# Kernel optimization log

Hardware: AMD Instinct MI355X
Metric: run time of the kernel (lower is better)

## Reference

```python
import jax, jax.numpy as jnp
import numpy as np

N_STEPS = 20      # max(n_steps_al, n_steps_kc)
ALPHA   = 0.9     # membrane decay exp(-dt/tau_m)
V_TH    = 1.0     # spiking threshold
G_SOMA  = 0.3     # dendrite->axon coupling conductance (2-compartment KC)
APL_GAIN = 1.0    # graded APL gain
I_SCALE = 0.5     # graded ORN drive scale
BETA    = 10.0    # surrogate-gradient sharpness ('soft' sigmoid)

@jax.custom_vjp
def spike(x):
    return (x > 0).astype(x.dtype)

def _spike_fwd(x):
    return spike(x), x

def _spike_bwd(x, g):
    s = jax.nn.sigmoid(BETA * x)
    return (g * BETA * s * (1.0 - s),)

spike.defvjp(_spike_fwd, _spike_bwd)


def _sparse_w(key, shape, density):
    k1, k2 = jax.random.split(key)
    mask = jax.random.bernoulli(k1, density, shape)
    w = jax.random.uniform(k2, shape)
    return (mask * w).astype(jnp.float32)


def setup_inputs() -> dict:
    key = jax.random.key(0)
    ks = jax.random.split(key, 10)
    batch, n_or, n_orn, n_ln, n_pn, n_kc, n_odors = 4096, 21, 42, 56, 42, 2000, 34
    or_input = jax.random.uniform(ks[0], (batch, n_or), dtype=jnp.float32)
    or_gains = jnp.ones((n_or,), jnp.float32)
    # fixed OR->ORN mapping: OR i drives left (2i) and right (2i+1) ORNs
    m = np.zeros((n_or, n_orn), np.float32)
    for i in range(n_or):
        m[i, 2 * i] = 1.0
        m[i, 2 * i + 1] = 1.0
    mapping = jnp.asarray(m)
    orn_to_pn = _sparse_w(ks[1], (n_orn, n_pn), 0.3)
    orn_to_ln = _sparse_w(ks[2], (n_orn, n_ln), 0.3)
    ln_to_pn = _sparse_w(ks[3], (n_ln, n_pn), 0.3)
    pn_to_kc = _sparse_w(ks[4], (n_pn, n_kc), 0.15)  # ~6 PN claws per KC
    kc_to_apl = jax.random.uniform(ks[5], (n_kc, 1), dtype=jnp.float32) * 0.01
    apl_to_kc = jax.random.uniform(ks[6], (1, n_kc), dtype=jnp.float32)
    dec_w = jax.random.normal(ks[7], (n_kc, n_odors), dtype=jnp.float32) * 0.02
    dec_b = jnp.zeros((n_odors,), jnp.float32)
    return {"or_input": or_input, "or_gains": or_gains, "mapping": mapping,
            "orn_to_pn": orn_to_pn, "orn_to_ln": orn_to_ln, "ln_to_pn": ln_to_pn,
            "pn_to_kc": pn_to_kc, "kc_to_apl": kc_to_apl, "apl_to_kc": apl_to_kc,
            "dec_w": dec_w, "dec_b": dec_b}


def reference(or_input, or_gains, mapping, orn_to_pn, orn_to_ln, ln_to_pn,
              pn_to_kc, kc_to_apl, apl_to_kc, dec_w, dec_b):
    B = or_input.shape[0]
    n_orn, n_pn = orn_to_pn.shape
    n_ln = orn_to_ln.shape[1]
    n_kc = pn_to_kc.shape[1]
    # OR transduction: graded, learnable per-OR gain
    orn_drive = (or_input * jax.nn.softplus(or_gains)) @ mapping  # [B, n_orn]

    z = lambda n: jnp.zeros((B, n), or_input.dtype)
    carry0 = (z(n_orn), z(n_ln), z(n_pn), z(n_kc), z(n_kc), z(1), z(n_kc))

    def step(carry, _):
        v_orn, v_ln, v_pn, v_d, v_a, apl, kc_cnt = carry
        # ORN LIF driven by graded OR current
        v_orn = ALPHA * v_orn + I_SCALE * orn_drive
        s_orn = spike(v_orn - V_TH)
        v_orn = v_orn * (1.0 - s_orn)
        # LN LIF (lateral inhibition interneurons)
        v_ln = ALPHA * v_ln + s_orn @ orn_to_ln
        s_ln = spike(v_ln - V_TH)
        v_ln = v_ln * (1.0 - s_ln)
        # PN LIF: ORN excitation, LN inhibition
        v_pn = ALPHA * v_pn + s_orn @ orn_to_pn - s_ln @ ln_to_pn
        s_pn = spike(v_pn - V_TH)
        v_pn = v_pn * (1.0 - s_pn)
        # KC 2-compartment: dendrite gets PN input and APL inhibition
        v_d = ALPHA * v_d + s_pn @ pn_to_kc - apl @ apl_to_kc
        v_a = ALPHA * v_a + G_SOMA * (v_d - v_a)
        s_kc = spike(v_a - V_TH)
        v_a = v_a * (1.0 - s_kc)
        # APL: graded (non-spiking) global inhibition from KC spikes
        apl = APL_GAIN * jax.nn.relu(s_kc @ kc_to_apl)
        return (v_orn, v_ln, v_pn, v_d, v_a, apl, kc_cnt + s_kc), None

    carry, _ = jax.lax.scan(step, carry0, None, length=N_STEPS)
    kc_count = carry[-1]
    kc_rates = kc_count / N_STEPS
    logits = kc_rates @ dec_w + dec_b  # [B, n_odors]
    return logits
```

## Files before the change

### kernel.cpp

```cpp
#include <hip/hip_runtime.h>

#define NSTEPS 20
#define ALPHA  0.9f
#define VTH    1.0f
#define GSOMA  0.3f
#define ISCALE 0.5f

#define NOR  21
#define NORN 42
#define NLN  56
#define NPN  42
#define NKC  2000
#define NOD  34

#define TPB  256
#define KPER 8

__global__ __launch_bounds__(TPB)
void phase1_sparse(const float* __restrict__ or_input,
                   const float* __restrict__ or_gains,
                   const float* __restrict__ mapping,
                   const float* __restrict__ orn_to_ln,
                   const float* __restrict__ orn_to_pn,
                   const float* __restrict__ ln_to_pn,
                   unsigned long long* __restrict__ gPN,
                   int batch)
{
    __shared__ float sOl[NORN * NLN];
    __shared__ float sOp[NORN * NPN];
    __shared__ float sLp[NLN * NPN];

    const int tid = threadIdx.x;
    for (int i = tid; i < NORN * NLN; i += TPB) sOl[i] = orn_to_ln[i];
    for (int i = tid; i < NORN * NPN; i += TPB) sOp[i] = orn_to_pn[i];
    for (int i = tid; i < NLN * NPN;  i += TPB) sLp[i] = ln_to_pn[i];
    __syncthreads();

    const int lane = tid & 63;
    const int wid  = tid >> 6;
    const int row  = blockIdx.x * 4 + wid;
    if (row >= batch) return;

    float spg = 0.f;
    if (lane < NOR) spg = log1pf(expf(or_gains[lane]));

    float drive = 0.f;
    {
        const float* x = or_input + (long)row * NOR;
        const int jo = lane < NORN ? lane : 0;
#pragma unroll
        for (int i = 0; i < NOR; ++i) {
            float g = __shfl(spg, i);
            drive += x[i] * g * mapping[i * NORN + jo];
        }
        drive *= ISCALE;
    }

    const int jl = lane < NLN ? lane : 0;
    const int jp = lane < NPN ? lane : 0;

    float v_orn = 0.f, v_ln = 0.f, v_pn = 0.f;
    unsigned long long* outm = gPN + (long)row * NSTEPS;

    for (int t = 0; t < NSTEPS; ++t) {
        bool so = false;
        if (lane < NORN) {
            v_orn = ALPHA * v_orn + drive;
            so = (v_orn - VTH) > 0.f;
            if (so) v_orn = 0.f;
        }
        unsigned long long mO = __ballot(so);

        float aln = 0.f, apn = 0.f;
        {
            unsigned long long m = mO;
            while (m) {
                const int p = __builtin_ctzll(m);
                m &= m - 1;
                aln += sOl[p * NLN + jl];
                apn += sOp[p * NPN + jp];
            }
        }

        bool sl = false;
        if (lane < NLN) {
            v_ln = ALPHA * v_ln + aln;
            sl = (v_ln - VTH) > 0.f;
            if (sl) v_ln = 0.f;
        }
        unsigned long long mL = __ballot(sl);

        float h = 0.f;
        {
            unsigned long long m = mL;
            while (m) {
                const int l = __builtin_ctzll(m);
                m &= m - 1;
                h += sLp[l * NPN + jp];
            }
        }

        bool sp = false;
        if (lane < NPN) {
            v_pn = ALPHA * v_pn + apn - h;
            sp = (v_pn - VTH) > 0.f;
            if (sp) v_pn = 0.f;
        }
        const unsigned long long mP = __ballot(sp);
        if (lane == 0) outm[t] = mP;
    }
}

__global__ __launch_bounds__(TPB)
void phase2_kernel(const unsigned long long* __restrict__ g_masks,
                   const float* __restrict__ pn_to_kc,
                   const float* __restrict__ kc_to_apl,
                   const float* __restrict__ apl_to_kc,
                   const float* __restrict__ dec_w,
                   const float* __restrict__ dec_b,
                   float* __restrict__ out)
{
    __shared__ float sRed[2][4];
    __shared__ float sRed2[4 * NOD];

    const int tid  = threadIdx.x;
    const int lane = tid & 63;
    const int wid  = tid >> 6;
    const int b    = blockIdx.x;

    const int  kbase = tid * KPER;
    const bool act   = (kbase < NKC);
    float vd[KPER], va[KPER], cnt[KPER], wa2k[KPER], wk2a[KPER];
#pragma unroll
    for (int j = 0; j < KPER; ++j) { vd[j] = 0.f; va[j] = 0.f; cnt[j] = 0.f; }
    {
        const float4* a4 = (const float4*)(apl_to_kc + (act ? kbase : 0));
        const float4* k4 = (const float4*)(kc_to_apl + (act ? kbase : 0));
        float4 a0 = a4[0], a1 = a4[1], k0 = k4[0], k1 = k4[1];
        const float g = act ? 1.f : 0.f;
        wa2k[0] = g * a0.x; wa2k[1] = g * a0.y; wa2k[2] = g * a0.z; wa2k[3] = g * a0.w;
        wa2k[4] = g * a1.x; wa2k[5] = g * a1.y; wa2k[6] = g * a1.z; wa2k[7] = g * a1.w;
        wk2a[0] = g * k0.x; wk2a[1] = g * k0.y; wk2a[2] = g * k0.z; wk2a[3] = g * k0.w;
        wk2a[4] = g * k1.x; wk2a[5] = g * k1.y; wk2a[6] = g * k1.z; wk2a[7] = g * k1.w;
    }
    if (tid < 8) sRed[tid >> 2][tid & 3] = 0.f;
    __syncthreads();

    const unsigned long long* gm = g_masks + (long)b * NSTEPS;

    for (int t = 0; t < NSTEPS; ++t) {
        const float* rp = sRed[(t + 1) & 1];
        const float apl = fmaxf(rp[0] + rp[1] + rp[2] + rp[3], 0.f);

#pragma unroll
        for (int j = 0; j < KPER; ++j) vd[j] = ALPHA * vd[j] - apl * wa2k[j];

        unsigned long long m = gm[t];
        while (m) {
            const int p0 = __builtin_ctzll(m); m &= m - 1;
            int p1 = p0; float f1 = 0.f;
            if (m) { p1 = __builtin_ctzll(m); m &= m - 1; f1 = 1.f; }
            if (act) {
                const float4* w0 = (const float4*)(pn_to_kc + (long)p0 * NKC + kbase);
                const float4* w1 = (const float4*)(pn_to_kc + (long)p1 * NKC + kbase);
                float4 a0 = w0[0], a1 = w0[1];
                float4 b0 = w1[0], b1 = w1[1];
                vd[0] += a0.x; vd[1] += a0.y; vd[2] += a0.z; vd[3] += a0.w;
                vd[4] += a1.x; vd[5] += a1.y; vd[6] += a1.z; vd[7] += a1.w;
                vd[0] += f1 * b0.x; vd[1] += f1 * b0.y; vd[2] += f1 * b0.z; vd[3] += f1 * b0.w;
                vd[4] += f1 * b1.x; vd[5] += f1 * b1.y; vd[6] += f1 * b1.z; vd[7] += f1 * b1.w;
            }
        }

        float aplp = 0.f;
#pragma unroll
        for (int j = 0; j < KPER; ++j) {
            va[j] = ALPHA * va[j] + GSOMA * (vd[j] - va[j]);
            float s = (va[j] - VTH) > 0.f ? 1.f : 0.f;
            va[j] *= (1.f - s);
            cnt[j] += s;
            aplp += s * wk2a[j];
        }
        for (int off = 32; off > 0; off >>= 1) aplp += __shfl_xor(aplp, off, 64);
        if (lane == 0) sRed[t & 1][wid] = aplp;
        __syncthreads();
    }

    float acc[NOD];
#pragma unroll
    for (int o = 0; o < NOD; ++o) acc[o] = 0.f;
    if (act) {
#pragma unroll
        for (int j = 0; j < KPER; ++j) {
            float r = cnt[j] / 20.0f;
            if (r != 0.f) {
                const float* wr = dec_w + (long)(kbase + j) * NOD;
#pragma unroll
                for (int o = 0; o < NOD; ++o) acc[o] += r * wr[o];
            }
        }
    }
#pragma unroll
    for (int o = 0; o < NOD; ++o) {
        float v = acc[o];
        for (int off = 32; off > 0; off >>= 1) v += __shfl_xor(v, off, 64);
        if (lane == 0) sRed2[wid * NOD + o] = v;
    }
    __syncthreads();
    if (tid < NOD) {
        float v = sRed2[tid] + sRed2[NOD + tid] + sRed2[2 * NOD + tid] +
                  sRed2[3 * NOD + tid] + dec_b[tid];
        out[(long)b * NOD + tid] = v;
    }
}

__global__ __launch_bounds__(TPB)
void snn_fused(const float* __restrict__ or_input, const float* __restrict__ or_gains,
               const float* __restrict__ mapping, const float* __restrict__ orn_to_pn,
               const float* __restrict__ orn_to_ln, const float* __restrict__ ln_to_pn,
               const float* __restrict__ pn_to_kc, const float* __restrict__ kc_to_apl,
               const float* __restrict__ apl_to_kc, const float* __restrict__ dec_w,
               const float* __restrict__ dec_b, float* __restrict__ out)
{
    __shared__ float sW_ol[NORN * NLN];
    __shared__ float sW_op[NORN * NPN];
    __shared__ float sW_lp[NLN * NPN];
    __shared__ float sDrive[NORN];
    __shared__ float sSpg[NOR];
    __shared__ float sOrn[NORN];
    __shared__ float sLn[NLN];
    __shared__ float sApl;
    __shared__ float sRed[4];
    __shared__ float sRed2[4 * NOD];
    __shared__ unsigned long long sMask;

    const int tid = threadIdx.x;
    const int b   = blockIdx.x;

    for (int i = tid; i < NORN * NLN; i += TPB) sW_ol[i] = orn_to_ln[i];
    for (int i = tid; i < NORN * NPN; i += TPB) sW_op[i] = orn_to_pn[i];
    for (int i = tid; i < NLN * NPN;  i += TPB) sW_lp[i] = ln_to_pn[i];
    if (tid < NOR) sSpg[tid] = log1pf(expf(or_gains[tid]));
    if (tid == 0)  sApl = 0.f;
    __syncthreads();

    if (tid < NORN) {
        const float* x = or_input + (long)b * NOR;
        float d = 0.f;
        for (int i = 0; i < NOR; ++i) d += x[i] * sSpg[i] * mapping[i * NORN + tid];
        sDrive[tid] = d * ISCALE;
    }

    const int  kbase = tid * KPER;
    const bool act   = (kbase < NKC);
    float vd[KPER], va[KPER], cnt[KPER], wa2k[KPER], wk2a[KPER];
#pragma unroll
    for (int j = 0; j < KPER; ++j) {
        vd[j] = 0.f; va[j] = 0.f; cnt[j] = 0.f;
        wa2k[j] = act ? apl_to_kc[kbase + j] : 0.f;
        wk2a[j] = act ? kc_to_apl[kbase + j] : 0.f;
    }
    float v_orn = 0.f, v_ln = 0.f, v_pn = 0.f, v_pn_exc = 0.f;
    __syncthreads();

    for (int t = 0; t < NSTEPS; ++t) {
        if (tid < NORN) {
            v_orn = ALPHA * v_orn + sDrive[tid];
            float s = (v_orn - VTH) > 0.f ? 1.f : 0.f;
            v_orn *= (1.f - s);
            sOrn[tid] = s;
        }
        __syncthreads();
        if (tid < NLN) {
            float a = 0.f;
            for (int o = 0; o < NORN; ++o) a += sOrn[o] * sW_ol[o * NLN + tid];
            v_ln = ALPHA * v_ln + a;
            float s = (v_ln - VTH) > 0.f ? 1.f : 0.f;
            v_ln *= (1.f - s);
            sLn[tid] = s;
        } else if (tid >= 64 && tid < 64 + NPN) {
            const int j = tid - 64;
            float a = 0.f;
            for (int o = 0; o < NORN; ++o) a += sOrn[o] * sW_op[o * NPN + j];
            v_pn_exc = a;
        }
        __syncthreads();
        if (tid >= 64 && tid < 64 + NPN) {
            const int j = tid - 64;
            float inh = 0.f;
            for (int l = 0; l < NLN; ++l) inh += sLn[l] * sW_lp[l * NPN + j];
            v_pn = ALPHA * v_pn + v_pn_exc - inh;
            bool s = (v_pn - VTH) > 0.f;
            if (s) v_pn = 0.f;
            unsigned long long bal = __ballot(s);
            if (tid == 64) sMask = bal;
        }
        __syncthreads();
        {
            const float apl = sApl;
#pragma unroll
            for (int j = 0; j < KPER; ++j) vd[j] = ALPHA * vd[j] - apl * wa2k[j];
            unsigned long long m = sMask;
            while (m) {
                const int p = __builtin_ctzll(m);
                m &= m - 1;
                if (act) {
                    const float4* w = (const float4*)(pn_to_kc + (long)p * NKC + kbase);
                    float4 w0 = w[0], w1 = w[1];
                    vd[0] += w0.x; vd[1] += w0.y; vd[2] += w0.z; vd[3] += w0.w;
                    vd[4] += w1.x; vd[5] += w1.y; vd[6] += w1.z; vd[7] += w1.w;
                }
            }
            float aplp = 0.f;
#pragma unroll
            for (int j = 0; j < KPER; ++j) {
                va[j] = ALPHA * va[j] + GSOMA * (vd[j] - va[j]);
                float s = (va[j] - VTH) > 0.f ? 1.f : 0.f;
                va[j] *= (1.f - s);
                cnt[j] += s;
                aplp += s * wk2a[j];
            }
            for (int off = 32; off > 0; off >>= 1) aplp += __shfl_xor(aplp, off, 64);
            if ((tid & 63) == 0) sRed[tid >> 6] = aplp;
        }
        __syncthreads();
        if (tid == 0) {
            float a = sRed[0] + sRed[1] + sRed[2] + sRed[3];
            sApl = fmaxf(a, 0.f);
        }
    }

    float acc[NOD];
#pragma unroll
    for (int o = 0; o < NOD; ++o) acc[o] = 0.f;
    if (act) {
#pragma unroll
        for (int j = 0; j < KPER; ++j) {
            float r = cnt[j] / 20.0f;
            if (r != 0.f) {
                const float* wr = dec_w + (long)(kbase + j) * NOD;
#pragma unroll
                for (int o = 0; o < NOD; ++o) acc[o] += r * wr[o];
            }
        }
    }
#pragma unroll
    for (int o = 0; o < NOD; ++o) {
        float v = acc[o];
        for (int off = 32; off > 0; off >>= 1) v += __shfl_xor(v, off, 64);
        if ((tid & 63) == 0) sRed2[(tid >> 6) * NOD + o] = v;
    }
    __syncthreads();
    if (tid < NOD) {
        float v = sRed2[tid] + sRed2[NOD + tid] + sRed2[2 * NOD + tid] +
                  sRed2[3 * NOD + tid] + dec_b[tid];
        out[(long)b * NOD + tid] = v;
    }
}

extern "C" void kernel_launch(void* const* d_in, const int* in_sizes, int n_in,
                              void* d_out, int out_size, void* d_ws, size_t ws_size,
                              hipStream_t stream) {
    (void)n_in; (void)out_size;
    const float* or_input  = (const float*)d_in[0];
    const float* or_gains  = (const float*)d_in[1];
    const float* mapping   = (const float*)d_in[2];
    const float* orn_to_pn = (const float*)d_in[3];
    const float* orn_to_ln = (const float*)d_in[4];
    const float* ln_to_pn  = (const float*)d_in[5];
    const float* pn_to_kc  = (const float*)d_in[6];
    const float* kc_to_apl = (const float*)d_in[7];
    const float* apl_to_kc = (const float*)d_in[8];
    const float* dec_w     = (const float*)d_in[9];
    const float* dec_b     = (const float*)d_in[10];
    float* out = (float*)d_out;

    const int batch = in_sizes[0] / NOR;
    const size_t needPN = (size_t)batch * NSTEPS * sizeof(unsigned long long);

    if (ws_size >= needPN) {
        unsigned long long* gPN = (unsigned long long*)d_ws;
        hipLaunchKernelGGL(phase1_sparse, dim3((batch + 3) / 4), dim3(TPB), 0, stream,
                           or_input, or_gains, mapping, orn_to_ln, orn_to_pn, ln_to_pn,
                           gPN, batch);
        hipLaunchKernelGGL(phase2_kernel, dim3(batch), dim3(TPB), 0, stream,
                           gPN, pn_to_kc, kc_to_apl, apl_to_kc, dec_w, dec_b, out);
    } else {
        hipLaunchKernelGGL(snn_fused, dim3(batch), dim3(TPB), 0, stream,
                           or_input, or_gains, mapping, orn_to_pn, orn_to_ln,
                           ln_to_pn, pn_to_kc, kc_to_apl, apl_to_kc, dec_w, dec_b, out);
    }
}
```

Measured before the change: 224.1 us.

## Fuse both phases into one warp-specialized kernel with producer wave pipelining

Replaces the two-kernel scheme, a phase-1 kernel that wrote PN spike masks to workspace and a phase-2 kernel that read them, with a single kernel of 320 threads per batch row. Wave 0 runs the ORN/LN/PN recurrence one step ahead and hands each PN mask to the four KC waves through a double-buffered shared slot. The producer's sparse bit loops become fully unrolled branch-free masked sums. This removes the workspace round trip and one launch, but every block now reloads the small weight matrices into shared memory. The larger block may also lower occupancy.

```diff
diff --git a/kernel.cpp b/kernel.cpp
--- a/kernel.cpp
+++ b/kernel.cpp
@@ -13,106 +13,16 @@
 #define NKC  2000
 #define NOD  34
 
-#define TPB  256
+#define TPB2 320
 #define KPER 8
 
-__global__ __launch_bounds__(TPB)
-void phase1_sparse(const float* __restrict__ or_input,
+__global__ __launch_bounds__(TPB2)
+void snn_pipelined(const float* __restrict__ or_input,
                    const float* __restrict__ or_gains,
                    const float* __restrict__ mapping,
+                   const float* __restrict__ orn_to_pn,
                    const float* __restrict__ orn_to_ln,
-                   const float* __restrict__ orn_to_pn,
                    const float* __restrict__ ln_to_pn,
-                   unsigned long long* __restrict__ gPN,
-                   int batch)
-{
-    __shared__ float sOl[NORN * NLN];
-    __shared__ float sOp[NORN * NPN];
-    __shared__ float sLp[NLN * NPN];
-
-    const int tid = threadIdx.x;
-    for (int i = tid; i < NORN * NLN; i += TPB) sOl[i] = orn_to_ln[i];
-    for (int i = tid; i < NORN * NPN; i += TPB) sOp[i] = orn_to_pn[i];
-    for (int i = tid; i < NLN * NPN;  i += TPB) sLp[i] = ln_to_pn[i];
-    __syncthreads();
-
-    const int lane = tid & 63;
-    const int wid  = tid >> 6;
-    const int row  = blockIdx.x * 4 + wid;
-    if (row >= batch) return;
-
-    float spg = 0.f;
-    if (lane < NOR) spg = log1pf(expf(or_gains[lane]));
-
-    float drive = 0.f;
-    {
-        const float* x = or_input + (long)row * NOR;
-        const int jo = lane < NORN ? lane : 0;
-#pragma unroll
-        for (int i = 0; i < NOR; ++i) {
-            float g = __shfl(spg, i);
-            drive += x[i] * g * mapping[i * NORN + jo];
-        }
-        drive *= ISCALE;
-    }
-
-    const int jl = lane < NLN ? lane : 0;
-    const int jp = lane < NPN ? lane : 0;
-
-    float v_orn = 0.f, v_ln = 0.f, v_pn = 0.f;
-    unsigned long long* outm = gPN + (long)row * NSTEPS;
-
-    for (int t = 0; t < NSTEPS; ++t) {
-        bool so = false;
-        if (lane < NORN) {
-            v_orn = ALPHA * v_orn + drive;
-            so = (v_orn - VTH) > 0.f;
-            if (so) v_orn = 0.f;
-        }
-        unsigned long long mO = __ballot(so);
-
-        float aln = 0.f, apn = 0.f;
-        {
-            unsigned long long m = mO;
-            while (m) {
-                const int p = __builtin_ctzll(m);
-                m &= m - 1;
-                aln += sOl[p * NLN + jl];
-                apn += sOp[p * NPN + jp];
-            }
-        }
-
-        bool sl = false;
-        if (lane < NLN) {
-            v_ln = ALPHA * v_ln + aln;
-            sl = (v_ln - VTH) > 0.f;
-            if (sl) v_ln = 0.f;
-        }
-        unsigned long long mL = __ballot(sl);
-
-        float h = 0.f;
-        {
-            unsigned long long m = mL;
-            while (m) {
-                const int l = __builtin_ctzll(m);
-                m &= m - 1;
-                h += sLp[l * NPN + jp];
-            }
-        }
-
-        bool sp = false;
-        if (lane < NPN) {
-            v_pn = ALPHA * v_pn + apn - h;
-            sp = (v_pn - VTH) > 0.f;
-            if (sp) v_pn = 0.f;
-        }
-        const unsigned long long mP = __ballot(sp);
-        if (lane == 0) outm[t] = mP;
-    }
-}
-
-__global__ __launch_bounds__(TPB)
-void phase2_kernel(const unsigned long long* __restrict__ g_masks,
                    const float* __restrict__ pn_to_kc,
                    const float* __restrict__ kc_to_apl,
                    const float* __restrict__ apl_to_kc,
@@ -120,22 +30,33 @@
                    const float* __restrict__ dec_b,
                    float* __restrict__ out)
 {
+    __shared__ float sOl[NORN * NLN];
+    __shared__ float sOp[NORN * NPN];
+    __shared__ float sLp[NLN * NPN];
     __shared__ float sRed[2][4];
     __shared__ float sRed2[4 * NOD];
+    __shared__ unsigned long long sMaskBuf[2];
 
     const int tid  = threadIdx.x;
     const int lane = tid & 63;
     const int wid  = tid >> 6;
     const int b    = blockIdx.x;
 
-    const int  kbase = tid * KPER;
-    const bool act   = (kbase < NKC);
+    for (int i = tid; i < NORN * NLN; i += TPB2) sOl[i] = orn_to_ln[i];
+    for (int i = tid; i < NORN * NPN; i += TPB2) sOp[i] = orn_to_pn[i];
+    for (int i = tid; i < NLN * NPN;  i += TPB2) sLp[i] = ln_to_pn[i];
+    if (tid < 8) sRed[tid >> 2][tid & 3] = 0.f;
+
+    const int  ctid  = tid - 64;
+    const int  kbase = ctid * KPER;
+    const bool act   = (tid >= 64) && (kbase < NKC);
     float vd[KPER], va[KPER], cnt[KPER], wa2k[KPER], wk2a[KPER];
 #pragma unroll
     for (int j = 0; j < KPER; ++j) { vd[j] = 0.f; va[j] = 0.f; cnt[j] = 0.f; }
     {
-        const float4* a4 = (const float4*)(apl_to_kc + (act ? kbase : 0));
-        const float4* k4 = (const float4*)(kc_to_apl + (act ? kbase : 0));
+        const int idx = act ? kbase : 0;
+        const float4* a4 = (const float4*)(apl_to_kc + idx);
+        const float4* k4 = (const float4*)(kc_to_apl + idx);
         float4 a0 = a4[0], a1 = a4[1], k0 = k4[0], k1 = k4[1];
         const float g = act ? 1.f : 0.f;
         wa2k[0] = g * a0.x; wa2k[1] = g * a0.y; wa2k[2] = g * a0.z; wa2k[3] = g * a0.w;
@@ -143,174 +64,111 @@
         wk2a[0] = g * k0.x; wk2a[1] = g * k0.y; wk2a[2] = g * k0.z; wk2a[3] = g * k0.w;
         wk2a[4] = g * k1.x; wk2a[5] = g * k1.y; wk2a[6] = g * k1.z; wk2a[7] = g * k1.w;
     }
-    if (tid < 8) sRed[tid >> 2][tid & 3] = 0.f;
+
+    float v_orn = 0.f, v_ln = 0.f, v_pn = 0.f, drive = 0.f;
+    const int jl = lane < NLN ? lane : 0;
+    const int jp = lane < NPN ? lane : 0;
+    if (wid == 0) {
+        float spg = 0.f;
+        if (lane < NOR) spg = log1pf(expf(or_gains[lane]));
+        const float* x = or_input + (long)b * NOR;
+        const int jo = lane < NORN ? lane : 0;
+#pragma unroll
+        for (int i = 0; i < NOR; ++i) {
+            float g = __shfl(spg, i);
+            drive += x[i] * g * mapping[i * NORN + jo];
+        }
+        drive *= ISCALE;
+    }
     __syncthreads();
 
-    const unsigned long long* gm = g_masks + (long)b * NSTEPS;
+#define PRODUCER_STEP(MP_OUT)                                                        \
+    {                                                                                \
+        bool so = false;                                                             \
+        if (lane < NORN) {                                                           \
+            v_orn = ALPHA * v_orn + drive;                                           \
+            so = (v_orn - VTH) > 0.f;                                                \
+            if (so) v_orn = 0.f;                                                     \
+        }                                                                            \
+        const unsigned long long mO = __ballot(so);                                  \
+        const unsigned int mo_lo = (unsigned int)mO;                                 \
+        const unsigned int mo_hi = (unsigned int)(mO >> 32);                         \
+        float aln = 0.f, apn = 0.f;                                                  \
+        _Pragma("unroll")                                                            \
+        for (int o = 0; o < 32; ++o) {                                               \
+            const float bit = (float)((mo_lo >> o) & 1u);                            \
+            aln += bit * sOl[o * NLN + jl];                                          \
+            apn += bit * sOp[o * NPN + jp];                                          \
+        }                                                                            \
+        _Pragma("unroll")                                                            \
+        for (int o = 32; o < NORN; ++o) {                                            \
+            const float bit = (float)((mo_hi >> (o - 32)) & 1u);                     \
+            aln += bit * sOl[o * NLN + jl];                                          \
+            apn += bit * sOp[o * NPN + jp];                                          \
+        }                                                                            \
+        bool sl = false;                                                             \
+        if (lane < NLN) {                                                            \
+            v_ln = ALPHA * v_ln + aln;                                               \
+            sl = (v_ln - VTH) > 0.f;                                                 \
+            if (sl) v_ln = 0.f;                                                      \
+        }                                                                            \
+        const unsigned long long mL = __ballot(sl);                                  \
+        const unsigned int ml_lo = (unsigned int)mL;                                 \
+        const unsigned int ml_hi = (unsigned int)(mL >> 32);                         \
+        float h = 0.f;                                                               \
+        _Pragma("unroll")                                                            \
+        for (int l = 0; l < 32; ++l)                                                 \
+            h += (float)((ml_lo >> l) & 1u) * sLp[l * NPN + jp];                     \
+        _Pragma("unroll")                                                            \
+        for (int l = 32; l < NLN; ++l)                                               \
+            h += (float)((ml_hi >> (l - 32)) & 1u) * sLp[l * NPN + jp];              \
+        bool sp = false;                                                             \
+        if (lane < NPN) {                                                            \
+            v_pn = ALPHA * v_pn + apn - h;                                           \
+            sp = (v_pn - VTH) > 0.f;                                                 \
+            if (sp) v_pn = 0.f;                                                      \
+        }                                                                            \
+        MP_OUT = __ballot(sp);                                                       \
+    }
+
+    if (wid == 0) {
+        unsigned long long mP;
+        PRODUCER_STEP(mP)
+        if (lane == 0) sMaskBuf[0] = mP;
+    }
+    __syncthreads();
 
     for (int t = 0; t < NSTEPS; ++t) {
-        const float* rp = sRed[(t + 1) & 1];
-        const float apl = fmaxf(rp[0] + rp[1] + rp[2] + rp[3], 0.f);
-
-#pragma unroll
-        for (int j = 0; j < KPER; ++j) vd[j] = ALPHA * vd[j] - apl * wa2k[j];
-
-        unsigned long long m = gm[t];
-        while (m) {
-            const int p0 = __builtin_ctzll(m); m &= m - 1;
-            int p1 = p0; float f1 = 0.f;
-            if (m) { p1 = __builtin_ctzll(m); m &= m - 1; f1 = 1.f; }
-            if (act) {
-                const float4* w0 = (const float4*)(pn_to_kc + (long)p0 * NKC + kbase);
-                const float4* w1 = (const float4*)(pn_to_kc + (long)p1 * NKC + kbase);
-                float4 a0 = w0[0], a1 = w0[1];
-                float4 b0 = w1[0], b1 = w1[1];
-                vd[0] += a0.x; vd[1] += a0.y; vd[2] += a0.z; vd[3] += a0.w;
-                vd[4] += a1.x; vd[5] += a1.y; vd[6] += a1.z; vd[7] += a1.w;
-                vd[0] += f1 * b0.x; vd[1] += f1 * b0.y; vd[2] += f1 * b0.z; vd[3] += f1 * b0.w;
-                vd[4] += f1 * b1.x; vd[5] += f1 * b1.y; vd[6] += f1 * b1.z; vd[7] += f1 * b1.w;
-            }
-        }
-
-        float aplp = 0.f;
-#pragma unroll
-        for (int j = 0; j < KPER; ++j) {
-            va[j] = ALPHA * va[j] + GSOMA * (vd[j] - va[j]);
-            float s = (va[j] - VTH) > 0.f ? 1.f : 0.f;
-            va[j] *= (1.f - s);
-            cnt[j] += s;
-            aplp += s * wk2a[j];
-        }
-        for (int off = 32; off > 0; off >>= 1) aplp += __shfl_xor(aplp, off, 64);
-        if (lane == 0) sRed[t & 1][wid] = aplp;
-        __syncthreads();
-    }
-
-    float acc[NOD];
-#pragma unroll
-    for (int o = 0; o < NOD; ++o) acc[o] = 0.f;
-    if (act) {
-#pragma unroll
-        for (int j = 0; j < KPER; ++j) {
-            float r = cnt[j] / 20.0f;
-            if (r != 0.f) {
-                const float* wr = dec_w + (long)(kbase + j) * NOD;
-#pragma unroll
-                for (int o = 0; o < NOD; ++o) acc[o] += r * wr[o];
-            }
-        }
-    }
-#pragma unroll
-    for (int o = 0; o < NOD; ++o) {
-        float v = acc[o];
-        for (int off = 32; off > 0; off >>= 1) v += __shfl_xor(v, off, 64);
-        if (lane == 0) sRed2[wid * NOD + o] = v;
-    }
-    __syncthreads();
-    if (tid < NOD) {
-        float v = sRed2[tid] + sRed2[NOD + tid] + sRed2[2 * NOD + tid] +
-                  sRed2[3 * NOD + tid] + dec_b[tid];
-        out[(long)b * NOD + tid] = v;
-    }
-}
-
-__global__ __launch_bounds__(TPB)
-void snn_fused(const float* __restrict__ or_input, const float* __restrict__ or_gains,
-               const float* __restrict__ mapping, const float* __restrict__ orn_to_pn,
-               const float* __restrict__ orn_to_ln, const float* __restrict__ ln_to_pn,
-               const float* __restrict__ pn_to_kc, const float* __restrict__ kc_to_apl,
-               const float* __restrict__ apl_to_kc, const float* __restrict__ dec_w,
-               const float* __restrict__ dec_b, float* __restrict__ out)
-{
-    __shared__ float sW_ol[NORN * NLN];
-    __shared__ float sW_op[NORN * NPN];
-    __shared__ float sW_lp[NLN * NPN];
-    __shared__ float sDrive[NORN];
-    __shared__ float sSpg[NOR];
-    __shared__ float sOrn[NORN];
-    __shared__ float sLn[NLN];
-    __shared__ float sApl;
-    __shared__ float sRed[4];
-    __shared__ float sRed2[4 * NOD];
-    __shared__ unsigned long long sMask;
-
-    const int tid = threadIdx.x;
-    const int b   = blockIdx.x;
-
-    for (int i = tid; i < NORN * NLN; i += TPB) sW_ol[i] = orn_to_ln[i];
-    for (int i = tid; i < NORN * NPN; i += TPB) sW_op[i] = orn_to_pn[i];
-    for (int i = tid; i < NLN * NPN;  i += TPB) sW_lp[i] = ln_to_pn[i];
-    if (tid < NOR) sSpg[tid] = log1pf(expf(or_gains[tid]));
-    if (tid == 0)  sApl = 0.f;
-    __syncthreads();
-
-    if (tid < NORN) {
-        const float* x = or_input + (long)b * NOR;
-        float d = 0.f;
-        for (int i = 0; i < NOR; ++i) d += x[i] * sSpg[i] * mapping[i * NORN + tid];
-        sDrive[tid] = d * ISCALE;
-    }
-
-    const int  kbase = tid * KPER;
-    const bool act   = (kbase < NKC);
-    float vd[KPER], va[KPER], cnt[KPER], wa2k[KPER], wk2a[KPER];
-#pragma unroll
-    for (int j = 0; j < KPER; ++j) {
-        vd[j] = 0.f; va[j] = 0.f; cnt[j] = 0.f;
-        wa2k[j] = act ? apl_to_kc[kbase + j] : 0.f;
-        wk2a[j] = act ? kc_to_apl[kbase + j] : 0.f;
-    }
-    float v_orn = 0.f, v_ln = 0.f, v_pn = 0.f, v_pn_exc = 0.f;
-    __syncthreads();
-
-    for (int t = 0; t < NSTEPS; ++t) {
-        if (tid < NORN) {
-            v_orn = ALPHA * v_orn + sDrive[tid];
-            float s = (v_orn - VTH) > 0.f ? 1.f : 0.f;
-            v_orn *= (1.f - s);
-            sOrn[tid] = s;
-        }
-        __syncthreads();
-        if (tid < NLN) {
-            float a = 0.f;
-            for (int o = 0; o < NORN; ++o) a += sOrn[o] * sW_ol[o * NLN + tid];
-            v_ln = ALPHA * v_ln + a;
-            float s = (v_ln - VTH) > 0.f ? 1.f : 0.f;
-            v_ln *= (1.f - s);
-            sLn[tid] = s;
-        } else if (tid >= 64 && tid < 64 + NPN) {
-            const int j = tid - 64;
-            float a = 0.f;
-            for (int o = 0; o < NORN; ++o) a += sOrn[o] * sW_op[o * NPN + j];
-            v_pn_exc = a;
-        }
-        __syncthreads();
-        if (tid >= 64 && tid < 64 + NPN) {
-            const int j = tid - 64;
-            float inh = 0.f;
-            for (int l = 0; l < NLN; ++l) inh += sLn[l] * sW_lp[l * NPN + j];
-            v_pn = ALPHA * v_pn + v_pn_exc - inh;
-            bool s = (v_pn - VTH) > 0.f;
-            if (s) v_pn = 0.f;
-            unsigned long long bal = __ballot(s);
-            if (tid == 64) sMask = bal;
-        }
-        __syncthreads();
-        {
-            const float apl = sApl;
+        if (wid == 0) {
+            if (t < NSTEPS - 1) {
+                unsigned long long mP;
+                PRODUCER_STEP(mP)
+                if (lane == 0) sMaskBuf[(t + 1) & 1] = mP;
+            }
+        } else {
+            const float* rp = sRed[(t + 1) & 1];
+            const float apl = fmaxf(rp[0] + rp[1] + rp[2] + rp[3], 0.f);
+
 #pragma unroll
             for (int j = 0; j < KPER; ++j) vd[j] = ALPHA * vd[j] - apl * wa2k[j];
-            unsigned long long m = sMask;
+
+            unsigned long long m = sMaskBuf[t & 1];
             while (m) {
-                const int p = __builtin_ctzll(m);
-                m &= m - 1;
+                const int p0 = __builtin_ctzll(m); m &= m - 1;
+                int p1 = p0; float f1 = 0.f;
+                if (m) { p1 = __builtin_ctzll(m); m &= m - 1; f1 = 1.f; }
                 if (act) {
-                    const float4* w = (const float4*)(pn_to_kc + (long)p * NKC + kbase);
-                    float4 w0 = w[0], w1 = w[1];
-                    vd[0] += w0.x; vd[1] += w0.y; vd[2] += w0.z; vd[3] += w0.w;
-                    vd[4] += w1.x; vd[5] += w1.y; vd[6] += w1.z; vd[7] += w1.w;
+                    const float4* w0 = (const float4*)(pn_to_kc + (long)p0 * NKC + kbase);
+                    const float4* w1 = (const float4*)(pn_to_kc + (long)p1 * NKC + kbase);
+                    float4 a0 = w0[0], a1 = w0[1];
+                    float4 b0 = w1[0], b1 = w1[1];
+                    vd[0] += a0.x; vd[1] += a0.y; vd[2] += a0.z; vd[3] += a0.w;
+                    vd[4] += a1.x; vd[5] += a1.y; vd[6] += a1.z; vd[7] += a1.w;
+                    vd[0] += f1 * b0.x; vd[1] += f1 * b0.y; vd[2] += f1 * b0.z; vd[3] += f1 * b0.w;
+                    vd[4] += f1 * b1.x; vd[5] += f1 * b1.y; vd[6] += f1 * b1.z; vd[7] += f1 * b1.w;
                 }
             }
+
             float aplp = 0.f;
 #pragma unroll
             for (int j = 0; j < KPER; ++j) {
@@ -321,34 +179,32 @@
                 aplp += s * wk2a[j];
             }
             for (int off = 32; off > 0; off >>= 1) aplp += __shfl_xor(aplp, off, 64);
-            if ((tid & 63) == 0) sRed[tid >> 6] = aplp;
+            if (lane == 0) sRed[t & 1][wid - 1] = aplp;
         }
         __syncthreads();
-        if (tid == 0) {
-            float a = sRed[0] + sRed[1] + sRed[2] + sRed[3];
-            sApl = fmaxf(a, 0.f);
-        }
-    }
-
-    float acc[NOD];
-#pragma unroll
-    for (int o = 0; o < NOD; ++o) acc[o] = 0.f;
-    if (act) {
-#pragma unroll
-        for (int j = 0; j < KPER; ++j) {
-            float r = cnt[j] / 20.0f;
-            if (r != 0.f) {
-                const float* wr = dec_w + (long)(kbase + j) * NOD;
-#pragma unroll
-                for (int o = 0; o < NOD; ++o) acc[o] += r * wr[o];
-            }
-        }
-    }
-#pragma unroll
-    for (int o = 0; o < NOD; ++o) {
-        float v = acc[o];
-        for (int off = 32; off > 0; off >>= 1) v += __shfl_xor(v, off, 64);
-        if ((tid & 63) == 0) sRed2[(tid >> 6) * NOD + o] = v;
+    }
+
+    if (wid >= 1) {
+        float acc[NOD];
+#pragma unroll
+        for (int o = 0; o < NOD; ++o) acc[o] = 0.f;
+        if (act) {
+#pragma unroll
+            for (int j = 0; j < KPER; ++j) {
+                float r = cnt[j] / 20.0f;
+                if (r != 0.f) {
+                    const float* wr = dec_w + (long)(kbase + j) * NOD;
+#pragma unroll
+                    for (int o = 0; o < NOD; ++o) acc[o] += r * wr[o];
+                }
+            }
+        }
+#pragma unroll
+        for (int o = 0; o < NOD; ++o) {
+            float v = acc[o];
+            for (int off = 32; off > 0; off >>= 1) v += __shfl_xor(v, off, 64);
+            if (lane == 0) sRed2[(wid - 1) * NOD + o] = v;
+        }
     }
     __syncthreads();
     if (tid < NOD) {
@@ -356,12 +212,13 @@
                   sRed2[3 * NOD + tid] + dec_b[tid];
         out[(long)b * NOD + tid] = v;
     }
+#undef PRODUCER_STEP
 }
 
 extern "C" void kernel_launch(void* const* d_in, const int* in_sizes, int n_in,
                               void* d_out, int out_size, void* d_ws, size_t ws_size,
                               hipStream_t stream) {
-    (void)n_in; (void)out_size;
+    (void)n_in; (void)out_size; (void)d_ws; (void)ws_size;
     const float* or_input  = (const float*)d_in[0];
     const float* or_gains  = (const float*)d_in[1];
     const float* mapping   = (const float*)d_in[2];
@@ -376,18 +233,8 @@
     float* out = (float*)d_out;
 
     const int batch = in_sizes[0] / NOR;
-    const size_t needPN = (size_t)batch * NSTEPS * sizeof(unsigned long long);
-
-    if (ws_size >= needPN) {
-        unsigned long long* gPN = (unsigned long long*)d_ws;
-        hipLaunchKernelGGL(phase1_sparse, dim3((batch + 3) / 4), dim3(TPB), 0, stream,
-                           or_input, or_gains, mapping, orn_to_ln, orn_to_pn, ln_to_pn,
-                           gPN, batch);
-        hipLaunchKernelGGL(phase2_kernel, dim3(batch), dim3(TPB), 0, stream,
-                           gPN, pn_to_kc, kc_to_apl, apl_to_kc, dec_w, dec_b, out);
-    } else {
-        hipLaunchKernelGGL(snn_fused, dim3(batch), dim3(TPB), 0, stream,
-                           or_input, or_gains, mapping, orn_to_pn, orn_to_ln,
-                           ln_to_pn, pn_to_kc, kc_to_apl, apl_to_kc, dec_w, dec_b, out);
-    }
+
+    hipLaunchKernelGGL(snn_pipelined, dim3(batch), dim3(TPB2), 0, stream,
+                       or_input, or_gains, mapping, orn_to_pn, orn_to_ln, ln_to_pn,
+                       pn_to_kc, kc_to_apl, apl_to_kc, dec_w, dec_b, out);
 }
```

After: 772.0 us. 3.44x slower.
